# Kernel optimization log

Hardware: AMD Instinct MI355X
Metric: run time of the kernel (lower is better)

Reference implementation:

```python
import jax, jax.numpy as jnp
import numpy as np

D_MODEL = 1024
NUM_HEADS = 16
HEAD_DIM = D_MODEL // NUM_HEADS
LN_EPS = 1e-3  # keras LayerNormalization default epsilon


def setup_inputs() -> dict:
    key = jax.random.key(0)
    ks = jax.random.split(key, 10)
    B, T = 2, 2048
    s = 1.0 / np.sqrt(D_MODEL)
    return {
        "x": jax.random.normal(ks[0], (B, T, D_MODEL), dtype=jnp.float32),
        "Wq": jax.random.normal(ks[1], (D_MODEL, D_MODEL), dtype=jnp.float32) * s,
        "Wk": jax.random.normal(ks[2], (D_MODEL, D_MODEL), dtype=jnp.float32) * s,
        "Wv": jax.random.normal(ks[3], (D_MODEL, D_MODEL), dtype=jnp.float32) * s,
        "Wg": jax.random.normal(ks[4], (D_MODEL, D_MODEL), dtype=jnp.float32) * s,
        "bg": jnp.zeros((D_MODEL,), dtype=jnp.float32),
        "Wo": jax.random.normal(ks[5], (D_MODEL, D_MODEL), dtype=jnp.float32) * s,
        "bo": jnp.zeros((D_MODEL,), dtype=jnp.float32),
        "ln_gamma": jnp.ones((D_MODEL,), dtype=jnp.float32),
        "ln_beta": jnp.zeros((D_MODEL,), dtype=jnp.float32),
    }


def reference(x, Wq, Wk, Wv, Wg, bg, Wo, bo, ln_gamma, ln_beta):
    B, T, D = x.shape
    H, dh = NUM_HEADS, HEAD_DIM

    def split_heads(z):
        return z.reshape(B, T, H, dh).transpose(0, 2, 1, 3)  # [B,H,T,dh]

    Q = split_heads(x @ Wq)
    K = split_heads(x @ Wk)
    V = split_heads(x @ Wv)
    G = jax.nn.swish(x @ Wg + bg)  # [B,T,D]

    # Per-head causal decay mask D[h,m,n] = gamma_h^(m-n) for m>=n else 0
    idx = jnp.arange(T, dtype=jnp.float32)
    diff = idx[:, None] - idx[None, :]  # [T,T]
    causal = (diff >= 0).astype(jnp.float32)
    gammas = 1.0 - 2.0 ** (-5.0 - jnp.arange(H, dtype=jnp.float32))  # [H]
    Dmask = (gammas[:, None, None] ** jnp.maximum(diff, 0.0)) * causal  # [H,T,T]

    scale = float(dh) ** 0.5
    scores = jnp.einsum('bhtd,bhsd->bhts', Q, K) / scale  # [B,H,T,T]
    ret = jnp.einsum('bhts,bhsd->bhtd', scores * Dmask[None], V)  # [B,H,T,dh]
    ret = ret.transpose(0, 2, 1, 3).reshape(B, T, D)  # concat heads

    # LayerNorm (axis=-1, keras default eps=1e-3)
    mu = jnp.mean(ret, axis=-1, keepdims=True)
    var = jnp.mean(jnp.square(ret - mu), axis=-1, keepdims=True)
    ln = (ret - mu) / jnp.sqrt(var + LN_EPS) * ln_gamma + ln_beta

    return (ln * G) @ Wo + bo
```

## Files before the change

### kernel.cpp

```cpp
#include <hip/hip_runtime.h>

#define D_MODEL 1024
#define NHEADS  16
#define HDIM    64
#define BATCH   2
#define SEQ     2048
#define ROWS    (BATCH*SEQ)
#define CHUNK   128
#define NCHUNK  (SEQ/CHUNK)
#define LN_EPS  1e-3f

typedef unsigned short ushort_t;
typedef __attribute__((ext_vector_type(4))) float          f32x4;
typedef __attribute__((ext_vector_type(8))) short          s16x8;
typedef __attribute__((ext_vector_type(4))) unsigned short u16x4;
typedef __attribute__((ext_vector_type(8))) unsigned short u16x8;

__device__ __forceinline__ ushort_t f2b(float f) {
    union { float f; unsigned int u; } v; v.f = f;
    unsigned int r = v.u + 0x7fffu + ((v.u >> 16) & 1u);
    return (ushort_t)(r >> 16);
}
__device__ __forceinline__ float b2f(ushort_t b) {
    union { unsigned int u; float f; } v; v.u = ((unsigned int)b) << 16;
    return v.f;
}

__device__ __forceinline__ void async_load16(const ushort_t* g, ushort_t* l) {
    __builtin_amdgcn_global_load_lds(
        (const __attribute__((address_space(1))) unsigned int*)(g),
        (__attribute__((address_space(3))) unsigned int*)(l),
        16, 0, 0);
}

__global__ __launch_bounds__(256) void prep_kernel(
        const float* __restrict__ x,
        const float* __restrict__ Wq, const float* __restrict__ Wk,
        const float* __restrict__ Wv, const float* __restrict__ Wg,
        const float* __restrict__ Wo,
        ushort_t* __restrict__ xb, ushort_t* __restrict__ WcatT,
        ushort_t* __restrict__ WoT) {
    __shared__ float tile[32][33];
    int bid = blockIdx.x, t = threadIdx.x;
    if (bid < 4096) {
        int idx = (bid * 256 + t) * 4;
        f32x4 v = *(const f32x4*)(x + idx);
        u16x4 o;
        o.x = f2b(v.x); o.y = f2b(v.y); o.z = f2b(v.z); o.w = f2b(v.w);
        *(u16x4*)(xb + idx) = o;
        return;
    }
    int zb = bid - 4096;
    int z = zb >> 10;
    int rem = zb & 1023;
    int bx = rem & 31, by = rem >> 5;
    const float* W = (z == 0) ? Wq : (z == 1) ? Wk : (z == 2) ? Wv : (z == 3) ? Wg : Wo;
    ushort_t* dst = (z < 4) ? (WcatT + (size_t)z * 1024 * 1024) : WoT;
    int n0 = bx * 32, k0 = by * 32;
    int tx = t & 31, ty = t >> 5;
#pragma unroll
    for (int i = 0; i < 4; i++) {
        int k = k0 + ty + i * 8;
        tile[ty + i * 8][tx] = W[(size_t)k * 1024 + n0 + tx];
    }
    __syncthreads();
#pragma unroll
    for (int i = 0; i < 4; i++) {
        int n = n0 + ty + i * 8;
        dst[(size_t)n * 1024 + k0 + tx] = f2b(tile[tx][ty + i * 8]);
    }
}

__global__ __launch_bounds__(256, 2) void gemm_kernel(
        const ushort_t* __restrict__ A, const ushort_t* __restrict__ BT,
        int K, int N, int mode, const float* __restrict__ bias,
        ushort_t* __restrict__ Yout, float* __restrict__ Fout) {
    extern __shared__ char smem[];
    ushort_t* As = (ushort_t*)smem;
    ushort_t* Bs = As + 128 * 64;
    int t = threadIdx.x;
    int row0 = blockIdx.y * 128, col0 = blockIdx.x * 128;
    int w = t >> 6, lane = t & 63;
    int wr = (w >> 1) * 64, wc = (w & 1) * 64;
    int qd = lane >> 4, ln = lane & 15;
    int lx = ln & 7;

    f32x4 acc[4][4];
#pragma unroll
    for (int i = 0; i < 4; i++)
#pragma unroll
        for (int j = 0; j < 4; j++) acc[i][j] = (f32x4)0.0f;

    for (int k0 = 0; k0 < K; k0 += 64) {
#pragma unroll
        for (int p = 0; p < 4; p++) {
            int g = p * 256 + t;
            int r = g >> 3;
            int kb = g & 7;
            int kbs = kb ^ (r & 7);
            async_load16(A + (size_t)(row0 + r) * K + k0 + kbs * 8, As + g * 8);
            async_load16(BT + (size_t)(col0 + r) * K + k0 + kbs * 8, Bs + g * 8);
        }
        __syncthreads();
#pragma unroll
        for (int kk = 0; kk < 64; kk += 32) {
            s16x8 af[4], bf[4];
            int kxa = ((kk >> 3) + qd) ^ lx;
#pragma unroll
            for (int i = 0; i < 4; i++)
                af[i] = *(const s16x8*)(As + (wr + i * 16 + ln) * 64 + kxa * 8);
#pragma unroll
            for (int j = 0; j < 4; j++)
                bf[j] = *(const s16x8*)(Bs + (wc + j * 16 + ln) * 64 + kxa * 8);
#pragma unroll
            for (int i = 0; i < 4; i++)
#pragma unroll
                for (int j = 0; j < 4; j++)
                    acc[i][j] = __builtin_amdgcn_mfma_f32_16x16x32_bf16(
                        af[i], bf[j], acc[i][j], 0, 0, 0);
        }
        __syncthreads();
    }

#pragma unroll
    for (int i = 0; i < 4; i++)
#pragma unroll
        for (int j = 0; j < 4; j++) {
            int n = col0 + wc + j * 16 + ln;
#pragma unroll
            for (int r = 0; r < 4; r++) {
                int m = row0 + wr + i * 16 + qd * 4 + r;
                float v = acc[i][j][r];
                if (mode == 0) {
                    int region = n >> 10;
                    if (region == 0) v *= 0.125f;
                    else if (region == 3) {
                        v += bias[n & 1023];
                        v = v / (1.0f + __expf(-v));
                    }
                    Yout[(size_t)m * N + n] = f2b(v);
                } else {
                    Fout[(size_t)m * N + n] = v + bias[n];
                }
            }
        }
}

#define SJ 136
__global__ __launch_bounds__(256) void chunk_states_kernel(const ushort_t* __restrict__ Y,
                                                           float* __restrict__ Astate) {
    __shared__ ushort_t Ktd[64 * SJ];
    __shared__ ushort_t Vtd[64 * SJ];
    int c = blockIdx.x, h = blockIdx.y, b = blockIdx.z;
    int t = threadIdx.x;
    float gamma = 1.0f - exp2f(-5.0f - (float)h);
    float l2g = log2f(gamma);
    int row0 = b * SEQ + c * CHUNK;
    int colK = D_MODEL + h * HDIM;

    {
        int dgi = t & 7, jg = t >> 3;
        u16x8 k8[4], v8[4];
        float dec[4];
#pragma unroll
        for (int r = 0; r < 4; r++) {
            int j = jg * 4 + r;
            size_t src = (size_t)(row0 + j) * 4096 + colK + dgi * 8;
            k8[r] = *(const u16x8*)(Y + src);
            v8[r] = *(const u16x8*)(Y + src + D_MODEL);
            dec[r] = exp2f((float)(127 - j) * l2g);
        }
#pragma unroll
        for (int q = 0; q < 8; q++) {
            int qq = q ^ dgi;
            u16x4 pk, pv;
#pragma unroll
            for (int r = 0; r < 4; r++) {
                pk[r] = f2b(b2f(k8[r][qq]) * dec[r]);
                pv[r] = v8[r][qq];
            }
            *(u16x4*)(Ktd + (dgi * 8 + qq) * SJ + jg * 4) = pk;
            *(u16x4*)(Vtd + (dgi * 8 + qq) * SJ + jg * 4) = pv;
        }
    }
    __syncthreads();

    int w = t >> 6, lane = t & 63;
    int wr = w * 16;
    int qd = lane >> 4, ln = lane & 15;

    s16x8 af[4];
#pragma unroll
    for (int ks = 0; ks < 4; ks++)
        af[ks] = *(const s16x8*)(Vtd + (wr + ln) * SJ + ks * 32 + qd * 8);

    f32x4 acc[4];
#pragma unroll
    for (int nt = 0; nt < 4; nt++) {
        acc[nt] = (f32x4)0.0f;
#pragma unroll
        for (int ks = 0; ks < 4; ks++) {
            s16x8 bf = *(const s16x8*)(Ktd + (nt * 16 + ln) * SJ + ks * 32 + qd * 8);
            acc[nt] = __builtin_amdgcn_mfma_f32_16x16x32_bf16(af[ks], bf, acc[nt], 0, 0, 0);
        }
    }

    size_t base = ((size_t)((b * NHEADS + h) * NCHUNK + c)) * 4096;
#pragma unroll
    for (int nt = 0; nt < 4; nt++)
#pragma unroll
        for (int r = 0; r < 4; r++)
            Astate[base + (size_t)(wr + qd * 4 + r) * 64 + nt * 16 + ln] = acc[nt][r];
}

__global__ __launch_bounds__(128) void scan_kernel(const float* __restrict__ Astate,
                                                   float* __restrict__ Sprev) {
    int h = blockIdx.x, b = blockIdx.y;
    int bh = b * NHEADS + h;
    float gamma = 1.0f - exp2f(-5.0f - (float)h);
    float gC = exp2f(128.0f * log2f(gamma));
    int g = blockIdx.z * 128 + threadIdx.x;
    size_t base = (size_t)bh * NCHUNK * 4096 + g * 4;
    f32x4 S = (f32x4)0.0f;
    for (int c = 0; c < NCHUNK; c++) {
        *(f32x4*)(Sprev + base + (size_t)c * 4096) = S;
        f32x4 Ain = *(const f32x4*)(Astate + base + (size_t)c * 4096);
        S = S * gC + Ain;
    }
}

#define LDW 72
#define VT_LDW 136
#define CO_ELEMS (128*LDW*2 + 64*LDW*2 + 64*VT_LDW)
__global__ __launch_bounds__(256, 2) void chunk_out_kernel(const ushort_t* __restrict__ Y,
                                                           const float* __restrict__ Sprev,
                                                           float* __restrict__ ret) {
    extern __shared__ char smem[];
    ushort_t* Qs   = (ushort_t*)smem;
    ushort_t* Kc   = Qs + 128 * LDW;
    ushort_t* Sphi = Kc + 128 * LDW;
    ushort_t* Splo = Sphi + 64 * LDW;
    ushort_t* Vt   = Splo + 64 * LDW;
    ushort_t* Pl   = Qs;

    int c = blockIdx.x, h = blockIdx.y, b = blockIdx.z;
    int t = threadIdx.x;
    float gamma = 1.0f - exp2f(-5.0f - (float)h);
    float l2g = log2f(gamma);
    int row0 = b * SEQ + c * CHUNK;

    for (int g = t; g < 1024; g += 256) {
        int i = g >> 3, dg = (g & 7) * 8;
        size_t src = (size_t)(row0 + i) * 4096 + h * HDIM + dg;
        *(u16x8*)(Qs + i * LDW + dg) = *(const u16x8*)(Y + src);
        *(u16x8*)(Kc + i * LDW + dg) = *(const u16x8*)(Y + src + D_MODEL);
    }
    {
        int dgi = t & 7, jg = t >> 3;
        u16x8 v8[4];
#pragma unroll
        for (int r = 0; r < 4; r++)
            v8[r] = *(const u16x8*)(Y + (size_t)(row0 + jg * 4 + r) * 4096
                                      + 2 * D_MODEL + h * HDIM + dgi * 8);
#pragma unroll
        for (int q = 0; q < 8; q++) {
            int qq = q ^ dgi;
            u16x4 pv;
#pragma unroll
            for (int r = 0; r < 4; r++) pv[r] = v8[r][qq];
            *(u16x4*)(Vt + (dgi * 8 + qq) * VT_LDW + jg * 4) = pv;
        }
    }
    {
        size_t sbase = ((size_t)((b * NHEADS + h) * NCHUNK + c)) * 4096;
        for (int g = t; g < 1024; g += 256) {
            int d = g >> 4, e0 = (g & 15) * 4;
            f32x4 s4 = *(const f32x4*)(Sprev + sbase + d * 64 + e0);
            u16x4 hi4, lo4;
#pragma unroll
            for (int k2 = 0; k2 < 4; k2++) {
                ushort_t hb = f2b(s4[k2]);
                hi4[k2] = hb;
                lo4[k2] = f2b(s4[k2] - b2f(hb));
            }
            *(u16x4*)(Sphi + d * LDW + e0) = hi4;
            *(u16x4*)(Splo + d * LDW + e0) = lo4;
        }
    }
    __syncthreads();

    int w = t >> 6, lane = t & 63;
    int wr = w * 32;
    int qd = lane >> 4, ln = lane & 15;

    s16x8 aq[2][2];
#pragma unroll
    for (int mt = 0; mt < 2; mt++)
#pragma unroll
        for (int ks = 0; ks < 2; ks++)
            aq[mt][ks] = *(const s16x8*)(Qs + (wr + mt * 16 + ln) * LDW + ks * 32 + qd * 8);

    float prow[2][4], pcolm[8];
#pragma unroll
    for (int mt = 0; mt < 2; mt++)
#pragma unroll
        for (int r = 0; r < 4; r++)
            prow[mt][r] = exp2f((float)(wr + mt * 16 + qd * 4 + r + 1) * l2g);
#pragma unroll
    for (int nt = 0; nt < 8; nt++)
        pcolm[nt] = exp2f(-(float)(nt * 16 + ln + 1) * l2g);

    f32x4 out[2][4];
#pragma unroll
    for (int mt = 0; mt < 2; mt++)
#pragma unroll
        for (int dt = 0; dt < 4; dt++) out[mt][dt] = (f32x4)0.0f;
#pragma unroll
    for (int dt = 0; dt < 4; dt++)
#pragma unroll
        for (int ks = 0; ks < 2; ks++) {
            s16x8 bh_ = *(const s16x8*)(Sphi + (dt * 16 + ln) * LDW + ks * 32 + qd * 8);
            s16x8 bl_ = *(const s16x8*)(Splo + (dt * 16 + ln) * LDW + ks * 32 + qd * 8);
#pragma unroll
            for (int mt = 0; mt < 2; mt++) {
                out[mt][dt] = __builtin_amdgcn_mfma_f32_16x16x32_bf16(
                    aq[mt][ks], bh_, out[mt][dt], 0, 0, 0);
                out[mt][dt] = __builtin_amdgcn_mfma_f32_16x16x32_bf16(
                    aq[mt][ks], bl_, out[mt][dt], 0, 0, 0);
            }
        }
#pragma unroll
    for (int mt = 0; mt < 2; mt++)
#pragma unroll
        for (int dt = 0; dt < 4; dt++)
#pragma unroll
            for (int r = 0; r < 4; r++) out[mt][dt][r] *= prow[mt][r];

    f32x4 sc[2][8];
#pragma unroll
    for (int mt = 0; mt < 2; mt++)
#pragma unroll
        for (int nt = 0; nt < 8; nt++) sc[mt][nt] = (f32x4)0.0f;
#pragma unroll
    for (int nt = 0; nt < 8; nt++)
#pragma unroll
        for (int ks = 0; ks < 2; ks++) {
            s16x8 bk = *(const s16x8*)(Kc + (nt * 16 + ln) * LDW + ks * 32 + qd * 8);
#pragma unroll
            for (int mt = 0; mt < 2; mt++)
                sc[mt][nt] = __builtin_amdgcn_mfma_f32_16x16x32_bf16(
                    aq[mt][ks], bk, sc[mt][nt], 0, 0, 0);
        }
    __syncthreads();

#pragma unroll
    for (int mt = 0; mt < 2; mt++)
#pragma unroll
        for (int nt = 0; nt < 8; nt++) {
            int j = nt * 16 + ln;
#pragma unroll
            for (int r = 0; r < 4; r++) {
                int i = wr + mt * 16 + qd * 4 + r;
                float v = (j <= i) ? sc[mt][nt][r] * (prow[mt][r] * pcolm[nt]) : 0.0f;
                Pl[i * VT_LDW + j] = f2b(v);
            }
        }
    __syncthreads();

#pragma unroll
    for (int ks = 0; ks < 4; ks++) {
        s16x8 ap[2];
#pragma unroll
        for (int mt = 0; mt < 2; mt++)
            ap[mt] = *(const s16x8*)(Pl + (wr + mt * 16 + ln) * VT_LDW + ks * 32 + qd * 8);
#pragma unroll
        for (int dt = 0; dt < 4; dt++) {
            s16x8 bv = *(const s16x8*)(Vt + (dt * 16 + ln) * VT_LDW + ks * 32 + qd * 8);
#pragma unroll
            for (int mt = 0; mt < 2; mt++)
                out[mt][dt] = __builtin_amdgcn_mfma_f32_16x16x32_bf16(
                    ap[mt], bv, out[mt][dt], 0, 0, 0);
        }
    }

#pragma unroll
    for (int mt = 0; mt < 2; mt++)
#pragma unroll
        for (int dt = 0; dt < 4; dt++)
#pragma unroll
            for (int r = 0; r < 4; r++) {
                int i = wr + mt * 16 + qd * 4 + r;
                ret[(size_t)(row0 + i) * D_MODEL + h * HDIM + dt * 16 + ln] = out[mt][dt][r];
            }
}

__global__ __launch_bounds__(256) void ln_gate_kernel(const float* __restrict__ ret,
                                                      const ushort_t* __restrict__ Y,
                                                      const float* __restrict__ lgam,
                                                      const float* __restrict__ lbet,
                                                      ushort_t* __restrict__ LNG) {
    int row = blockIdx.x, t = threadIdx.x;
    f32x4 v = *(const f32x4*)(ret + (size_t)row * D_MODEL + t * 4);
    float s  = v.x + v.y + v.z + v.w;
    float sq = v.x * v.x + v.y * v.y + v.z * v.z + v.w * v.w;
#pragma unroll
    for (int m = 1; m < 64; m <<= 1) {
        s  += __shfl_xor(s, m);
        sq += __shfl_xor(sq, m);
    }
    __shared__ float red[8];
    int w = t >> 6, lane = t & 63;
    if (lane == 0) { red[w * 2] = s; red[w * 2 + 1] = sq; }
    __syncthreads();
    s  = red[0] + red[2] + red[4] + red[6];
    sq = red[1] + red[3] + red[5] + red[7];
    float mu  = s * (1.0f / 1024.0f);
    float var = sq * (1.0f / 1024.0f) - mu * mu;
    float inv = rsqrtf(var + LN_EPS);
    int col = t * 4;
    u16x4 ug = *(const u16x4*)(Y + (size_t)row * 4096 + 3 * D_MODEL + col);
    u16x4 o;
    o.x = f2b(((v.x - mu) * inv * lgam[col + 0] + lbet[col + 0]) * b2f(ug.x));
    o.y = f2b(((v.y - mu) * inv * lgam[col + 1] + lbet[col + 1]) * b2f(ug.y));
    o.z = f2b(((v.z - mu) * inv * lgam[col + 2] + lbet[col + 2]) * b2f(ug.z));
    o.w = f2b(((v.w - mu) * inv * lgam[col + 3] + lbet[col + 3]) * b2f(ug.w));
    *(u16x4*)(LNG + (size_t)row * D_MODEL + col) = o;
}

extern "C" void kernel_launch(void* const* d_in, const int* in_sizes, int n_in,
                              void* d_out, int out_size, void* d_ws, size_t ws_size,
                              hipStream_t stream) {
    const float* x   = (const float*)d_in[0];
    const float* Wq  = (const float*)d_in[1];
    const float* Wk  = (const float*)d_in[2];
    const float* Wv  = (const float*)d_in[3];
    const float* Wg  = (const float*)d_in[4];
    const float* bg  = (const float*)d_in[5];
    const float* Wo  = (const float*)d_in[6];
    const float* bo  = (const float*)d_in[7];
    const float* lng = (const float*)d_in[8];
    const float* lnb = (const float*)d_in[9];
    float* out = (float*)d_out;

    char* ws = (char*)d_ws;
    ushort_t* xb    = (ushort_t*)(ws);
    ushort_t* WcatT = (ushort_t*)(ws + (8ull  << 20));
    ushort_t* WoT   = (ushort_t*)(ws + (16ull << 20));
    ushort_t* Yb    = (ushort_t*)(ws + (18ull << 20));
    float*    retb  = (float*)   (ws + (50ull << 20));
    float*    Ast   = (float*)   (ws + (66ull << 20));
    float*    Sprv  = (float*)   (ws + (74ull << 20));
    ushort_t* LNGb  = (ushort_t*)(ws + (82ull << 20));

    const int GEMM_LDS = 2 * 128 * 64 * 2;
    const int CO_BYTES = CO_ELEMS * 2;

    hipFuncSetAttribute(reinterpret_cast<const void*>(gemm_kernel),
                        hipFuncAttributeMaxDynamicSharedMemorySize, GEMM_LDS);
    hipFuncSetAttribute(reinterpret_cast<const void*>(chunk_out_kernel),
                        hipFuncAttributeMaxDynamicSharedMemorySize, CO_BYTES);

    prep_kernel<<<4096 + 5120, 256, 0, stream>>>(x, Wq, Wk, Wv, Wg, Wo, xb, WcatT, WoT);

    gemm_kernel<<<dim3(32, 32), 256, GEMM_LDS, stream>>>(
        xb, WcatT, 1024, 4096, 0, bg, Yb, (float*)nullptr);

    chunk_states_kernel<<<dim3(NCHUNK, NHEADS, BATCH), 256, 0, stream>>>(Yb, Ast);
    scan_kernel<<<dim3(NHEADS, BATCH, 8), 128, 0, stream>>>(Ast, Sprv);
    chunk_out_kernel<<<dim3(NCHUNK, NHEADS, BATCH), 256, CO_BYTES, stream>>>(
        Yb, Sprv, retb);

    ln_gate_kernel<<<ROWS, 256, 0, stream>>>(retb, Yb, lng, lnb, LNGb);

    gemm_kernel<<<dim3(8, 32), 256, GEMM_LDS, stream>>>(
        LNGb, WoT, 1024, 1024, 1, bo, (ushort_t*)nullptr, out);
}
```

Before: 203.7 us.

## Fuse chunk states, scan and output into one retention kernel; fold LayerNorm into output GEMM

Replaces the chunk-state, scan and chunk-output kernels with a single retention kernel in which each block recomputes the decayed state from all preceding chunks in registers. Block order is reversed for the second batch to balance the uneven work. Row sums and sums of squares for LayerNorm are accumulated with atomics into a zeroed buffer, and the normalization and gating are applied while staging A tiles in the output GEMM. This drops two intermediate global buffers and three launches, at the cost of redundant quadratic state recomputation, since later chunks loop over up to 15 earlier chunks, and of a non-deterministic atomic reduction order.

```diff
diff --git a/kernel.cpp b/kernel.cpp
--- a/kernel.cpp
+++ b/kernel.cpp
@@ -39,10 +39,12 @@
         const float* __restrict__ Wv, const float* __restrict__ Wg,
         const float* __restrict__ Wo,
         ushort_t* __restrict__ xb, ushort_t* __restrict__ WcatT,
-        ushort_t* __restrict__ WoT) {
+        ushort_t* __restrict__ WoT, float* __restrict__ rowstats) {
     __shared__ float tile[32][33];
     int bid = blockIdx.x, t = threadIdx.x;
     if (bid < 4096) {
+        if (bid < 8)
+            *(f32x4*)(rowstats + (bid * 256 + t) * 4) = (f32x4)0.0f;
         int idx = (bid * 256 + t) * 4;
         f32x4 v = *(const f32x4*)(x + idx);
         u16x4 o;
@@ -73,8 +75,8 @@
 
 __global__ __launch_bounds__(256, 2) void gemm_kernel(
         const ushort_t* __restrict__ A, const ushort_t* __restrict__ BT,
-        int K, int N, int mode, const float* __restrict__ bias,
-        ushort_t* __restrict__ Yout, float* __restrict__ Fout) {
+        int K, int N, const float* __restrict__ bias,
+        ushort_t* __restrict__ Yout) {
     extern __shared__ char smem[];
     ushort_t* As = (ushort_t*)smem;
     ushort_t* Bs = As + 128 * 64;
@@ -127,114 +129,28 @@
 #pragma unroll
         for (int j = 0; j < 4; j++) {
             int n = col0 + wc + j * 16 + ln;
+            int region = n >> 10;
 #pragma unroll
             for (int r = 0; r < 4; r++) {
                 int m = row0 + wr + i * 16 + qd * 4 + r;
                 float v = acc[i][j][r];
-                if (mode == 0) {
-                    int region = n >> 10;
-                    if (region == 0) v *= 0.125f;
-                    else if (region == 3) {
-                        v += bias[n & 1023];
-                        v = v / (1.0f + __expf(-v));
-                    }
-                    Yout[(size_t)m * N + n] = f2b(v);
-                } else {
-                    Fout[(size_t)m * N + n] = v + bias[n];
+                if (region == 0) v *= 0.125f;
+                else if (region == 3) {
+                    v += bias[n & 1023];
+                    v = v / (1.0f + __expf(-v));
                 }
-            }
-        }
-}
-
+                Yout[(size_t)m * N + n] = f2b(v);
+            }
+        }
+}
+
+#define LDW 72
 #define SJ 136
-__global__ __launch_bounds__(256) void chunk_states_kernel(const ushort_t* __restrict__ Y,
-                                                           float* __restrict__ Astate) {
-    __shared__ ushort_t Ktd[64 * SJ];
-    __shared__ ushort_t Vtd[64 * SJ];
-    int c = blockIdx.x, h = blockIdx.y, b = blockIdx.z;
-    int t = threadIdx.x;
-    float gamma = 1.0f - exp2f(-5.0f - (float)h);
-    float l2g = log2f(gamma);
-    int row0 = b * SEQ + c * CHUNK;
-    int colK = D_MODEL + h * HDIM;
-
-    {
-        int dgi = t & 7, jg = t >> 3;
-        u16x8 k8[4], v8[4];
-        float dec[4];
-#pragma unroll
-        for (int r = 0; r < 4; r++) {
-            int j = jg * 4 + r;
-            size_t src = (size_t)(row0 + j) * 4096 + colK + dgi * 8;
-            k8[r] = *(const u16x8*)(Y + src);
-            v8[r] = *(const u16x8*)(Y + src + D_MODEL);
-            dec[r] = exp2f((float)(127 - j) * l2g);
-        }
-#pragma unroll
-        for (int q = 0; q < 8; q++) {
-            int qq = q ^ dgi;
-            u16x4 pk, pv;
-#pragma unroll
-            for (int r = 0; r < 4; r++) {
-                pk[r] = f2b(b2f(k8[r][qq]) * dec[r]);
-                pv[r] = v8[r][qq];
-            }
-            *(u16x4*)(Ktd + (dgi * 8 + qq) * SJ + jg * 4) = pk;
-            *(u16x4*)(Vtd + (dgi * 8 + qq) * SJ + jg * 4) = pv;
-        }
-    }
-    __syncthreads();
-
-    int w = t >> 6, lane = t & 63;
-    int wr = w * 16;
-    int qd = lane >> 4, ln = lane & 15;
-
-    s16x8 af[4];
-#pragma unroll
-    for (int ks = 0; ks < 4; ks++)
-        af[ks] = *(const s16x8*)(Vtd + (wr + ln) * SJ + ks * 32 + qd * 8);
-
-    f32x4 acc[4];
-#pragma unroll
-    for (int nt = 0; nt < 4; nt++) {
-        acc[nt] = (f32x4)0.0f;
-#pragma unroll
-        for (int ks = 0; ks < 4; ks++) {
-            s16x8 bf = *(const s16x8*)(Ktd + (nt * 16 + ln) * SJ + ks * 32 + qd * 8);
-            acc[nt] = __builtin_amdgcn_mfma_f32_16x16x32_bf16(af[ks], bf, acc[nt], 0, 0, 0);
-        }
-    }
-
-    size_t base = ((size_t)((b * NHEADS + h) * NCHUNK + c)) * 4096;
-#pragma unroll
-    for (int nt = 0; nt < 4; nt++)
-#pragma unroll
-        for (int r = 0; r < 4; r++)
-            Astate[base + (size_t)(wr + qd * 4 + r) * 64 + nt * 16 + ln] = acc[nt][r];
-}
-
-__global__ __launch_bounds__(128) void scan_kernel(const float* __restrict__ Astate,
-                                                   float* __restrict__ Sprev) {
-    int h = blockIdx.x, b = blockIdx.y;
-    int bh = b * NHEADS + h;
-    float gamma = 1.0f - exp2f(-5.0f - (float)h);
-    float gC = exp2f(128.0f * log2f(gamma));
-    int g = blockIdx.z * 128 + threadIdx.x;
-    size_t base = (size_t)bh * NCHUNK * 4096 + g * 4;
-    f32x4 S = (f32x4)0.0f;
-    for (int c = 0; c < NCHUNK; c++) {
-        *(f32x4*)(Sprev + base + (size_t)c * 4096) = S;
-        f32x4 Ain = *(const f32x4*)(Astate + base + (size_t)c * 4096);
-        S = S * gC + Ain;
-    }
-}
-
-#define LDW 72
 #define VT_LDW 136
 #define CO_ELEMS (128*LDW*2 + 64*LDW*2 + 64*VT_LDW)
-__global__ __launch_bounds__(256, 2) void chunk_out_kernel(const ushort_t* __restrict__ Y,
-                                                           const float* __restrict__ Sprev,
-                                                           float* __restrict__ ret) {
+__global__ __launch_bounds__(256, 2) void retention_kernel(const ushort_t* __restrict__ Y,
+                                                           float* __restrict__ ret,
+                                                           float* __restrict__ rowstats) {
     extern __shared__ char smem[];
     ushort_t* Qs   = (ushort_t*)smem;
     ushort_t* Kc   = Qs + 128 * LDW;
@@ -242,12 +158,98 @@
     ushort_t* Splo = Sphi + 64 * LDW;
     ushort_t* Vt   = Splo + 64 * LDW;
     ushort_t* Pl   = Qs;
-
-    int c = blockIdx.x, h = blockIdx.y, b = blockIdx.z;
+    ushort_t* Ktd  = Qs;
+    ushort_t* Vtd  = Ktd + 64 * SJ;
+
+    int c_raw = blockIdx.x, h = blockIdx.y, b = blockIdx.z;
+    int c = b ? (NCHUNK - 1 - c_raw) : c_raw;
     int t = threadIdx.x;
     float gamma = 1.0f - exp2f(-5.0f - (float)h);
     float l2g = log2f(gamma);
+    float gC = exp2f(128.0f * l2g);
     int row0 = b * SEQ + c * CHUNK;
+    int colK = D_MODEL + h * HDIM;
+
+    int w = t >> 6, lane = t & 63;
+    int wr = w * 16;
+    int qd = lane >> 4, ln = lane & 15;
+    int dgi = t & 7, jg = t >> 3;
+
+    {
+        u16x8 v8[4];
+#pragma unroll
+        for (int r = 0; r < 4; r++)
+            v8[r] = *(const u16x8*)(Y + (size_t)(row0 + jg * 4 + r) * 4096
+                                      + 2 * D_MODEL + h * HDIM + dgi * 8);
+#pragma unroll
+        for (int q = 0; q < 8; q++) {
+            int qq = q ^ dgi;
+            u16x4 pv;
+#pragma unroll
+            for (int r = 0; r < 4; r++) pv[r] = v8[r][qq];
+            *(u16x4*)(Vt + (dgi * 8 + qq) * VT_LDW + jg * 4) = pv;
+        }
+    }
+
+    f32x4 Sreg[4];
+#pragma unroll
+    for (int nt = 0; nt < 4; nt++) Sreg[nt] = (f32x4)0.0f;
+
+    for (int cp = 0; cp < c; cp++) {
+        int prow0 = b * SEQ + cp * CHUNK;
+        __syncthreads();
+        {
+            u16x8 k8[4], v8[4];
+            float dec[4];
+#pragma unroll
+            for (int r = 0; r < 4; r++) {
+                int j = jg * 4 + r;
+                size_t src = (size_t)(prow0 + j) * 4096 + colK + dgi * 8;
+                k8[r] = *(const u16x8*)(Y + src);
+                v8[r] = *(const u16x8*)(Y + src + D_MODEL);
+                dec[r] = exp2f((float)(127 - j) * l2g);
+            }
+#pragma unroll
+            for (int q = 0; q < 8; q++) {
+                int qq = q ^ dgi;
+                u16x4 pk, pv;
+#pragma unroll
+                for (int r = 0; r < 4; r++) {
+                    pk[r] = f2b(b2f(k8[r][qq]) * dec[r]);
+                    pv[r] = v8[r][qq];
+                }
+                *(u16x4*)(Ktd + (dgi * 8 + qq) * SJ + jg * 4) = pk;
+                *(u16x4*)(Vtd + (dgi * 8 + qq) * SJ + jg * 4) = pv;
+            }
+        }
+        __syncthreads();
+        s16x8 af[4];
+#pragma unroll
+        for (int ks = 0; ks < 4; ks++)
+            af[ks] = *(const s16x8*)(Vtd + (wr + ln) * SJ + ks * 32 + qd * 8);
+#pragma unroll
+        for (int nt = 0; nt < 4; nt++) {
+            f32x4 a4 = (f32x4)0.0f;
+#pragma unroll
+            for (int ks = 0; ks < 4; ks++) {
+                s16x8 bf = *(const s16x8*)(Ktd + (nt * 16 + ln) * SJ + ks * 32 + qd * 8);
+                a4 = __builtin_amdgcn_mfma_f32_16x16x32_bf16(af[ks], bf, a4, 0, 0, 0);
+            }
+            Sreg[nt] = Sreg[nt] * gC + a4;
+        }
+    }
+    __syncthreads();
+
+#pragma unroll
+    for (int nt = 0; nt < 4; nt++)
+#pragma unroll
+        for (int r = 0; r < 4; r++) {
+            int d = wr + qd * 4 + r, e = nt * 16 + ln;
+            float s = Sreg[nt][r];
+            ushort_t hb = f2b(s);
+            Sphi[d * LDW + e] = hb;
+            Splo[d * LDW + e] = f2b(s - b2f(hb));
+        }
 
     for (int g = t; g < 1024; g += 256) {
         int i = g >> 3, dg = (g & 7) * 8;
@@ -255,57 +257,23 @@
         *(u16x8*)(Qs + i * LDW + dg) = *(const u16x8*)(Y + src);
         *(u16x8*)(Kc + i * LDW + dg) = *(const u16x8*)(Y + src + D_MODEL);
     }
-    {
-        int dgi = t & 7, jg = t >> 3;
-        u16x8 v8[4];
+    __syncthreads();
+
+    int wr2 = w * 32;
+
+    s16x8 aq[2][2];
+#pragma unroll
+    for (int mt = 0; mt < 2; mt++)
+#pragma unroll
+        for (int ks = 0; ks < 2; ks++)
+            aq[mt][ks] = *(const s16x8*)(Qs + (wr2 + mt * 16 + ln) * LDW + ks * 32 + qd * 8);
+
+    float prow[2][4], pcolm[8];
+#pragma unroll
+    for (int mt = 0; mt < 2; mt++)
 #pragma unroll
         for (int r = 0; r < 4; r++)
-            v8[r] = *(const u16x8*)(Y + (size_t)(row0 + jg * 4 + r) * 4096
-                                      + 2 * D_MODEL + h * HDIM + dgi * 8);
-#pragma unroll
-        for (int q = 0; q < 8; q++) {
-            int qq = q ^ dgi;
-            u16x4 pv;
-#pragma unroll
-            for (int r = 0; r < 4; r++) pv[r] = v8[r][qq];
-            *(u16x4*)(Vt + (dgi * 8 + qq) * VT_LDW + jg * 4) = pv;
-        }
-    }
-    {
-        size_t sbase = ((size_t)((b * NHEADS + h) * NCHUNK + c)) * 4096;
-        for (int g = t; g < 1024; g += 256) {
-            int d = g >> 4, e0 = (g & 15) * 4;
-            f32x4 s4 = *(const f32x4*)(Sprev + sbase + d * 64 + e0);
-            u16x4 hi4, lo4;
-#pragma unroll
-            for (int k2 = 0; k2 < 4; k2++) {
-                ushort_t hb = f2b(s4[k2]);
-                hi4[k2] = hb;
-                lo4[k2] = f2b(s4[k2] - b2f(hb));
-            }
-            *(u16x4*)(Sphi + d * LDW + e0) = hi4;
-            *(u16x4*)(Splo + d * LDW + e0) = lo4;
-        }
-    }
-    __syncthreads();
-
-    int w = t >> 6, lane = t & 63;
-    int wr = w * 32;
-    int qd = lane >> 4, ln = lane & 15;
-
-    s16x8 aq[2][2];
-#pragma unroll
-    for (int mt = 0; mt < 2; mt++)
-#pragma unroll
-        for (int ks = 0; ks < 2; ks++)
-            aq[mt][ks] = *(const s16x8*)(Qs + (wr + mt * 16 + ln) * LDW + ks * 32 + qd * 8);
-
-    float prow[2][4], pcolm[8];
-#pragma unroll
-    for (int mt = 0; mt < 2; mt++)
-#pragma unroll
-        for (int r = 0; r < 4; r++)
-            prow[mt][r] = exp2f((float)(wr + mt * 16 + qd * 4 + r + 1) * l2g);
+            prow[mt][r] = exp2f((float)(wr2 + mt * 16 + qd * 4 + r + 1) * l2g);
 #pragma unroll
     for (int nt = 0; nt < 8; nt++)
         pcolm[nt] = exp2f(-(float)(nt * 16 + ln + 1) * l2g);
@@ -360,7 +328,7 @@
             int j = nt * 16 + ln;
 #pragma unroll
             for (int r = 0; r < 4; r++) {
-                int i = wr + mt * 16 + qd * 4 + r;
+                int i = wr2 + mt * 16 + qd * 4 + r;
                 float v = (j <= i) ? sc[mt][nt][r] * (prow[mt][r] * pcolm[nt]) : 0.0f;
                 Pl[i * VT_LDW + j] = f2b(v);
             }
@@ -372,7 +340,7 @@
         s16x8 ap[2];
 #pragma unroll
         for (int mt = 0; mt < 2; mt++)
-            ap[mt] = *(const s16x8*)(Pl + (wr + mt * 16 + ln) * VT_LDW + ks * 32 + qd * 8);
+            ap[mt] = *(const s16x8*)(Pl + (wr2 + mt * 16 + ln) * VT_LDW + ks * 32 + qd * 8);
 #pragma unroll
         for (int dt = 0; dt < 4; dt++) {
             s16x8 bv = *(const s16x8*)(Vt + (dt * 16 + ln) * VT_LDW + ks * 32 + qd * 8);
@@ -383,48 +351,138 @@
         }
     }
 
+    float psum[2][4], psq[2][4];
+#pragma unroll
+    for (int mt = 0; mt < 2; mt++)
+#pragma unroll
+        for (int r = 0; r < 4; r++) { psum[mt][r] = 0.0f; psq[mt][r] = 0.0f; }
 #pragma unroll
     for (int mt = 0; mt < 2; mt++)
 #pragma unroll
         for (int dt = 0; dt < 4; dt++)
 #pragma unroll
             for (int r = 0; r < 4; r++) {
-                int i = wr + mt * 16 + qd * 4 + r;
-                ret[(size_t)(row0 + i) * D_MODEL + h * HDIM + dt * 16 + ln] = out[mt][dt][r];
-            }
-}
-
-__global__ __launch_bounds__(256) void ln_gate_kernel(const float* __restrict__ ret,
-                                                      const ushort_t* __restrict__ Y,
-                                                      const float* __restrict__ lgam,
-                                                      const float* __restrict__ lbet,
-                                                      ushort_t* __restrict__ LNG) {
-    int row = blockIdx.x, t = threadIdx.x;
-    f32x4 v = *(const f32x4*)(ret + (size_t)row * D_MODEL + t * 4);
-    float s  = v.x + v.y + v.z + v.w;
-    float sq = v.x * v.x + v.y * v.y + v.z * v.z + v.w * v.w;
-#pragma unroll
-    for (int m = 1; m < 64; m <<= 1) {
-        s  += __shfl_xor(s, m);
-        sq += __shfl_xor(sq, m);
-    }
-    __shared__ float red[8];
+                int i = wr2 + mt * 16 + qd * 4 + r;
+                float v = out[mt][dt][r];
+                ret[(size_t)(row0 + i) * D_MODEL + h * HDIM + dt * 16 + ln] = v;
+                psum[mt][r] += v;
+                psq[mt][r]  += v * v;
+            }
+#pragma unroll
+    for (int m = 1; m < 16; m <<= 1)
+#pragma unroll
+        for (int mt = 0; mt < 2; mt++)
+#pragma unroll
+            for (int r = 0; r < 4; r++) {
+                psum[mt][r] += __shfl_xor(psum[mt][r], m);
+                psq[mt][r]  += __shfl_xor(psq[mt][r], m);
+            }
+    if (ln == 0) {
+#pragma unroll
+        for (int mt = 0; mt < 2; mt++)
+#pragma unroll
+            for (int r = 0; r < 4; r++) {
+                int i = row0 + wr2 + mt * 16 + qd * 4 + r;
+                atomicAdd(rowstats + 2 * i,     psum[mt][r]);
+                atomicAdd(rowstats + 2 * i + 1, psq[mt][r]);
+            }
+    }
+}
+
+__global__ __launch_bounds__(256, 2) void gemm2_ln_kernel(
+        const float* __restrict__ ret, const ushort_t* __restrict__ Y,
+        const float* __restrict__ rowstats, const ushort_t* __restrict__ BT,
+        const float* __restrict__ bo, const float* __restrict__ lgam,
+        const float* __restrict__ lbet, float* __restrict__ Fout) {
+    extern __shared__ char smem[];
+    ushort_t* As   = (ushort_t*)smem;
+    ushort_t* Bs   = As + 128 * 64;
+    float*    muv  = (float*)(Bs + 128 * 64);
+    float*    lnpg = muv + 256;
+    float*    lnpb = lnpg + 1024;
+    int t = threadIdx.x;
+    int row0 = blockIdx.y * 128, col0 = blockIdx.x * 128;
     int w = t >> 6, lane = t & 63;
-    if (lane == 0) { red[w * 2] = s; red[w * 2 + 1] = sq; }
+    int wr = (w >> 1) * 64, wc = (w & 1) * 64;
+    int qd = lane >> 4, ln = lane & 15;
+    int lx = ln & 7;
+
+    if (t < 128) {
+        float s  = rowstats[2 * (row0 + t)];
+        float sq = rowstats[2 * (row0 + t) + 1];
+        float mu = s * (1.0f / 1024.0f);
+        float var = sq * (1.0f / 1024.0f) - mu * mu;
+        muv[2 * t]     = mu;
+        muv[2 * t + 1] = rsqrtf(var + LN_EPS);
+    }
+    if (t < 256) {
+        *(f32x4*)(lnpg + t * 4) = *(const f32x4*)(lgam + t * 4);
+        *(f32x4*)(lnpb + t * 4) = *(const f32x4*)(lbet + t * 4);
+    }
     __syncthreads();
-    s  = red[0] + red[2] + red[4] + red[6];
-    sq = red[1] + red[3] + red[5] + red[7];
-    float mu  = s * (1.0f / 1024.0f);
-    float var = sq * (1.0f / 1024.0f) - mu * mu;
-    float inv = rsqrtf(var + LN_EPS);
-    int col = t * 4;
-    u16x4 ug = *(const u16x4*)(Y + (size_t)row * 4096 + 3 * D_MODEL + col);
-    u16x4 o;
-    o.x = f2b(((v.x - mu) * inv * lgam[col + 0] + lbet[col + 0]) * b2f(ug.x));
-    o.y = f2b(((v.y - mu) * inv * lgam[col + 1] + lbet[col + 1]) * b2f(ug.y));
-    o.z = f2b(((v.z - mu) * inv * lgam[col + 2] + lbet[col + 2]) * b2f(ug.z));
-    o.w = f2b(((v.w - mu) * inv * lgam[col + 3] + lbet[col + 3]) * b2f(ug.w));
-    *(u16x4*)(LNG + (size_t)row * D_MODEL + col) = o;
+
+    f32x4 acc[4][4];
+#pragma unroll
+    for (int i = 0; i < 4; i++)
+#pragma unroll
+        for (int j = 0; j < 4; j++) acc[i][j] = (f32x4)0.0f;
+
+    for (int k0 = 0; k0 < 1024; k0 += 64) {
+#pragma unroll
+        for (int p = 0; p < 4; p++) {
+            int g = p * 256 + t;
+            int r = g >> 3;
+            int kb = g & 7;
+            int kbs = kb ^ (r & 7);
+            int col = k0 + kbs * 8;
+            int m = row0 + r;
+            float mu = muv[2 * r], inv = muv[2 * r + 1];
+            f32x4 rv0 = *(const f32x4*)(ret + (size_t)m * 1024 + col);
+            f32x4 rv1 = *(const f32x4*)(ret + (size_t)m * 1024 + col + 4);
+            u16x8 gg = *(const u16x8*)(Y + (size_t)m * 4096 + 3 * D_MODEL + col);
+            f32x4 ga0 = *(const f32x4*)(lnpg + col),  ga1 = *(const f32x4*)(lnpg + col + 4);
+            f32x4 gb0 = *(const f32x4*)(lnpb + col),  gb1 = *(const f32x4*)(lnpb + col + 4);
+            u16x8 a;
+#pragma unroll
+            for (int q = 0; q < 4; q++) {
+                a[q]     = f2b(((rv0[q] - mu) * inv * ga0[q] + gb0[q]) * b2f(gg[q]));
+                a[q + 4] = f2b(((rv1[q] - mu) * inv * ga1[q] + gb1[q]) * b2f(gg[q + 4]));
+            }
+            *(u16x8*)(As + g * 8) = a;
+            async_load16(BT + (size_t)(col0 + r) * 1024 + k0 + kbs * 8, Bs + g * 8);
+        }
+        __syncthreads();
+#pragma unroll
+        for (int kk = 0; kk < 64; kk += 32) {
+            s16x8 af[4], bf[4];
+            int kxa = ((kk >> 3) + qd) ^ lx;
+#pragma unroll
+            for (int i = 0; i < 4; i++)
+                af[i] = *(const s16x8*)(As + (wr + i * 16 + ln) * 64 + kxa * 8);
+#pragma unroll
+            for (int j = 0; j < 4; j++)
+                bf[j] = *(const s16x8*)(Bs + (wc + j * 16 + ln) * 64 + kxa * 8);
+#pragma unroll
+            for (int i = 0; i < 4; i++)
+#pragma unroll
+                for (int j = 0; j < 4; j++)
+                    acc[i][j] = __builtin_amdgcn_mfma_f32_16x16x32_bf16(
+                        af[i], bf[j], acc[i][j], 0, 0, 0);
+        }
+        __syncthreads();
+    }
+
+#pragma unroll
+    for (int i = 0; i < 4; i++)
+#pragma unroll
+        for (int j = 0; j < 4; j++) {
+            int n = col0 + wc + j * 16 + ln;
+#pragma unroll
+            for (int r = 0; r < 4; r++) {
+                int m = row0 + wr + i * 16 + qd * 4 + r;
+                Fout[(size_t)m * 1024 + n] = acc[i][j][r] + bo[n];
+            }
+        }
 }
 
 extern "C" void kernel_launch(void* const* d_in, const int* in_sizes, int n_in,
@@ -448,30 +506,28 @@
     ushort_t* WoT   = (ushort_t*)(ws + (16ull << 20));
     ushort_t* Yb    = (ushort_t*)(ws + (18ull << 20));
     float*    retb  = (float*)   (ws + (50ull << 20));
-    float*    Ast   = (float*)   (ws + (66ull << 20));
-    float*    Sprv  = (float*)   (ws + (74ull << 20));
-    ushort_t* LNGb  = (ushort_t*)(ws + (82ull << 20));
+    float*    rstat = (float*)   (ws + (66ull << 20));
 
     const int GEMM_LDS = 2 * 128 * 64 * 2;
     const int CO_BYTES = CO_ELEMS * 2;
+    const int G2_LDS   = 2 * 128 * 64 * 2 + 256 * 4 + 2048 * 4;
 
     hipFuncSetAttribute(reinterpret_cast<const void*>(gemm_kernel),
                         hipFuncAttributeMaxDynamicSharedMemorySize, GEMM_LDS);
-    hipFuncSetAttribute(reinterpret_cast<const void*>(chunk_out_kernel),
+    hipFuncSetAttribute(reinterpret_cast<const void*>(retention_kernel),
                         hipFuncAttributeMaxDynamicSharedMemorySize, CO_BYTES);
-
-    prep_kernel<<<4096 + 5120, 256, 0, stream>>>(x, Wq, Wk, Wv, Wg, Wo, xb, WcatT, WoT);
+    hipFuncSetAttribute(reinterpret_cast<const void*>(gemm2_ln_kernel),
+                        hipFuncAttributeMaxDynamicSharedMemorySize, G2_LDS);
+
+    prep_kernel<<<4096 + 5120, 256, 0, stream>>>(x, Wq, Wk, Wv, Wg, Wo,
+                                                 xb, WcatT, WoT, rstat);
 
     gemm_kernel<<<dim3(32, 32), 256, GEMM_LDS, stream>>>(
-        xb, WcatT, 1024, 4096, 0, bg, Yb, (float*)nullptr);
-
-    chunk_states_kernel<<<dim3(NCHUNK, NHEADS, BATCH), 256, 0, stream>>>(Yb, Ast);
-    scan_kernel<<<dim3(NHEADS, BATCH, 8), 128, 0, stream>>>(Ast, Sprv);
-    chunk_out_kernel<<<dim3(NCHUNK, NHEADS, BATCH), 256, CO_BYTES, stream>>>(
-        Yb, Sprv, retb);
-
-    ln_gate_kernel<<<ROWS, 256, 0, stream>>>(retb, Yb, lng, lnb, LNGb);
-
-    gemm_kernel<<<dim3(8, 32), 256, GEMM_LDS, stream>>>(
-        LNGb, WoT, 1024, 1024, 1, bo, (ushort_t*)nullptr, out);
-}
+        xb, WcatT, 1024, 4096, bg, Yb);
+
+    retention_kernel<<<dim3(NCHUNK, NHEADS, BATCH), 256, CO_BYTES, stream>>>(
+        Yb, retb, rstat);
+
+    gemm2_ln_kernel<<<dim3(8, 32), 256, G2_LDS, stream>>>(
+        retb, Yb, rstat, WoT, bo, lng, lnb, out);
+}
```

Measured after the change: 271.3 us. +33.2%, slower.
